# Optimization experiments

Measured on AMD Instinct MI355X. Metric: run time of the kernel, lower is better.

## Reference

```python
import jax, jax.numpy as jnp
import numpy as np

B, T, D, H, C = 32, 160, 512, 256, 6625  # batch, time, feat, gru hidden, num classes


def _gru_scan(x_proj, rk, rbias):
    """Keras GRU (reset_after=True) over time.
    x_proj: [T, B, 3H] = x @ kernel + input_bias (precomputed).
    rk: [H, 3H] recurrent kernel, rbias: [3H] recurrent bias.
    Returns hidden states [T, B, H]."""
    h0 = jnp.zeros((x_proj.shape[1], rk.shape[0]), dtype=x_proj.dtype)

    def step(h, xp):
        inner = h @ rk + rbias                 # [B, 3H]
        xz, xr, xh = jnp.split(xp, 3, axis=-1)
        rz, rr, rh = jnp.split(inner, 3, axis=-1)
        z = jax.nn.sigmoid(xz + rz)            # update gate
        r = jax.nn.sigmoid(xr + rr)            # reset gate
        hh = jnp.tanh(xh + r * rh)             # candidate
        hn = z * h + (1.0 - z) * hh
        return hn, hn

    _, hs = jax.lax.scan(step, h0, x_proj)
    return hs  # [T, B, H]


def setup_inputs() -> dict:
    key = jax.random.key(0)
    ks = jax.random.split(key, 9)
    s_in, s_rec, s_cls = 1.0 / np.sqrt(D), 1.0 / np.sqrt(H), 0.1
    return {
        "x": jax.random.normal(ks[0], (B, T, D), jnp.float32),
        "kernel_fwd": jax.random.normal(ks[1], (D, 3 * H), jnp.float32) * s_in,
        "rk_fwd": jax.random.normal(ks[2], (H, 3 * H), jnp.float32) * s_rec,
        "bias_fwd": jnp.zeros((2, 3 * H), jnp.float32),
        "kernel_bwd": jax.random.normal(ks[3], (D, 3 * H), jnp.float32) * s_in,
        "rk_bwd": jax.random.normal(ks[4], (H, 3 * H), jnp.float32) * s_rec,
        "bias_bwd": jnp.zeros((2, 3 * H), jnp.float32),
        "W": jax.random.truncated_normal(ks[5], -2.0, 2.0, (2 * H, C), jnp.float32) * s_cls,
        "b": jnp.zeros((C,), jnp.float32),
    }


def reference(x, kernel_fwd, rk_fwd, bias_fwd, kernel_bwd, rk_bwd, bias_bwd, W, b):
    x_t = jnp.transpose(x, (1, 0, 2))                       # [T, B, D]
    # forward direction
    xp_f = x_t @ kernel_fwd + bias_fwd[0]                   # [T, B, 3H]
    h_f = _gru_scan(xp_f, rk_fwd, bias_fwd[1])              # [T, B, H]
    # backward direction: run on time-reversed input, reverse output
    x_rev = x_t[::-1]
    xp_b = x_rev @ kernel_bwd + bias_bwd[0]
    h_b = _gru_scan(xp_b, rk_bwd, bias_bwd[1])[::-1]        # [T, B, H]
    out = jnp.concatenate([h_f, h_b], axis=-1)              # [T, B, 2H]
    # classifier applied per position; original reshape/matmul/reshape/transpose
    # ([B,T,2H]->[-1,2H]@W -> [B,T,C] -> [T,B,C]) is equivalent to this:
    logits = out @ W + b                                    # [T, B, C]
    return logits
```

## Files before the change

### kernel.cpp

```cpp
#include <hip/hip_runtime.h>
#include <hip/hip_bf16.h>


#define B 32
#define T 160
#define D 512
#define H 256
#define C 6625
#define H3 768
#define NT16 416
#define KP_PER_DIR 393216
#define RKB_PER_DIR 196608

typedef __attribute__((ext_vector_type(8))) short short8v;
typedef __attribute__((ext_vector_type(4))) float float4v;

__device__ inline unsigned short f2bf(float v) {
    __hip_bfloat16 b = __float2bfloat16(v);
    return *reinterpret_cast<unsigned short*>(&b);
}
__device__ inline float bf2f(unsigned short u) {
    return __uint_as_float((unsigned int)u << 16);
}

__global__ __launch_bounds__(256) void pack_rkB_kernel(
    const float* __restrict__ rkf, const float* __restrict__ rkb,
    unsigned short* __restrict__ rkB)
{
    const int idx = blockIdx.x * 256 + threadIdx.x;
    const int dir = blockIdx.y;
    const float* rk = dir ? rkb : rkf;
    const int i   = idx & 7;
    const int col = (idx >> 3) & 15;
    const int kc  = (idx >> 7) & 31;
    const int nt  = idx >> 12;
    rkB[dir * RKB_PER_DIR + idx] = f2bf(rk[(kc * 8 + i) * H3 + nt * 16 + col]);
}

__global__ __launch_bounds__(256) void pack_W_kernel(
    const float* __restrict__ W, unsigned short* __restrict__ Wp)
{
    const int idx = blockIdx.x * 256 + threadIdx.x;
    const int i   = idx & 7;
    const int col = (idx >> 3) & 15;
    const int kc  = (idx >> 7) & 63;
    const int nt  = idx >> 13;
    const int k = kc * 8 + i;
    const int c = nt * 16 + col;
    const float v = (c < C) ? W[k * C + c] : 0.f;
    Wp[idx] = f2bf(v);
}

__global__ __launch_bounds__(256) void pack_xb_kernel(
    const float* __restrict__ x, unsigned short* __restrict__ xb)
{
    const int idx = blockIdx.x * 256 + threadIdx.x;
    const int k   = idx & 511;
    const int row = idx >> 9;
    const int t   = row >> 5;
    const int b   = row & 31;
    xb[idx] = f2bf(x[(b * T + t) * 512 + k]);
}

__global__ __launch_bounds__(256) void pack_kern_kernel(
    const float* __restrict__ kf, const float* __restrict__ kb,
    unsigned short* __restrict__ kernP)
{
    const int idx = blockIdx.x * 256 + threadIdx.x;
    const int dir = blockIdx.y;
    const float* kern = dir ? kb : kf;
    const int i   = idx & 7;
    const int col = (idx >> 3) & 15;
    const int kc  = (idx >> 7) & 63;
    const int nt  = idx >> 13;
    kernP[dir * KP_PER_DIR + idx] = f2bf(kern[(kc * 8 + i) * H3 + nt * 16 + col]);
}

__global__ __launch_bounds__(256) void proj_mfma_kernel(
    const unsigned short* __restrict__ xb,
    const unsigned short* __restrict__ kernP,
    const float* __restrict__ bias_f,
    const float* __restrict__ bias_b,
    unsigned short* __restrict__ xpb)
{
    const int bid = blockIdx.x;
    const int ct  = bid / 40;
    const int rt  = bid % 40;
    const int dir = blockIdx.y;
    const int lane = threadIdx.x & 63;
    const int wid  = threadIdx.x >> 6;
    const int wm = wid >> 1, wn = wid & 1;
    const int rowBase = rt * 128 + wm * 64;
    const int lrow = lane & 15;
    const int lk8  = lane >> 4;
    const float* bias = dir ? bias_b : bias_f;

    float4v acc[4][4];
#pragma unroll
    for (int i = 0; i < 4; ++i)
#pragma unroll
        for (int k = 0; k < 4; ++k) acc[i][k] = (float4v){0.f, 0.f, 0.f, 0.f};

    const short* A  = (const short*)xb;
    const short* Bp = (const short*)(kernP + dir * KP_PER_DIR);
    const int ntBase = ct * 8 + wn * 4;

    int arow[4];
#pragma unroll
    for (int mt = 0; mt < 4; ++mt) {
        const int r0 = rowBase + mt * 16;
        const int s  = r0 >> 5;
        arow[mt] = (dir ? (159 - s) : s) * 32 + (r0 & 31);
    }

    for (int k0 = 0; k0 < 512; k0 += 32) {
        short8v aF[4], bF[4];
#pragma unroll
        for (int mt = 0; mt < 4; ++mt)
            aF[mt] = *(const short8v*)&A[(arow[mt] + lrow) * 512 + k0 + lk8 * 8];
#pragma unroll
        for (int ntw = 0; ntw < 4; ++ntw)
            bF[ntw] = *(const short8v*)&Bp[((ntBase + ntw) * 64 + (k0 >> 3) + lk8) * 128 + lrow * 8];
#pragma unroll
        for (int mt = 0; mt < 4; ++mt)
#pragma unroll
            for (int ntw = 0; ntw < 4; ++ntw)
                acc[mt][ntw] = __builtin_amdgcn_mfma_f32_16x16x32_bf16(
                    aF[mt], bF[ntw], acc[mt][ntw], 0, 0, 0);
    }

    const int orow = (lane >> 4) * 4;
#pragma unroll
    for (int ntw = 0; ntw < 4; ++ntw) {
        const int c = (ntBase + ntw) * 16 + lrow;
        const float bc = bias[c];
#pragma unroll
        for (int mt = 0; mt < 4; ++mt)
#pragma unroll
            for (int v = 0; v < 4; ++v)
                xpb[(size_t)(dir * 5120 + rowBase + mt * 16 + orow + v) * H3 + c]
                    = f2bf(acc[mt][ntw][v] + bc);
    }
}

__global__ __launch_bounds__(768, 3) void gru_scan_v6(
    const unsigned short* __restrict__ xpb,
    const unsigned short* __restrict__ rkB,
    const float* __restrict__ bias_f,
    const float* __restrict__ bias_b,
    __hip_bfloat16* __restrict__ hcatb)
{
    const int bid = blockIdx.x;
    const int dir = bid >> 5;
    const int b   = bid & 31;
    const int tid = threadIdx.x;
    const int wv  = tid >> 6;
    const int lane = tid & 63;
    const int lrow = lane & 15;
    const int lk8  = lane >> 4;
    const int j   = tid & 255;
    const float* bias = dir ? bias_b : bias_f;
    const short* Bp = (const short*)(rkB + (size_t)dir * RKB_PER_DIR);

    short8v bw[32];
#pragma unroll
    for (int i = 0; i < 4; ++i)
#pragma unroll
        for (int kk = 0; kk < 8; ++kk)
            bw[i * 8 + kk] = *(const short8v*)
                &Bp[(((wv * 4 + i) * 32) + kk * 4 + lk8) * 128 + lrow * 8];

    float rbz = 0.f, rbr = 0.f, rbh = 0.f;
    if (tid < 256) {
        rbz = bias[H3 + j];
        rbr = bias[H3 + 256 + j];
        rbh = bias[H3 + 512 + j];
    }

    __shared__ float hfp[256];
    __shared__ __align__(16) unsigned short hus[256];
    __shared__ float sums[768];
    if (tid < 256) { hfp[tid] = 0.f; hus[tid] = 0; }
    __syncthreads();

    for (int s = 0; s < T; ++s) {
        float xz = 0.f, xr = 0.f, xh = 0.f;
        if (tid < 256) {
            const unsigned short* xrow = xpb + ((size_t)(dir * T + s) * B + b) * H3;
            xz = bf2f(xrow[j]);
            xr = bf2f(xrow[256 + j]);
            xh = bf2f(xrow[512 + j]);
        }

        float4v a0 = {0.f,0.f,0.f,0.f}, a1 = {0.f,0.f,0.f,0.f};
        float4v a2 = {0.f,0.f,0.f,0.f}, a3 = {0.f,0.f,0.f,0.f};
#pragma unroll
        for (int kk = 0; kk < 8; ++kk) {
            short8v aF = *(const short8v*)&hus[kk * 32 + lk8 * 8];
            a0 = __builtin_amdgcn_mfma_f32_16x16x32_bf16(aF, bw[0 * 8 + kk], a0, 0, 0, 0);
            a1 = __builtin_amdgcn_mfma_f32_16x16x32_bf16(aF, bw[1 * 8 + kk], a1, 0, 0, 0);
            a2 = __builtin_amdgcn_mfma_f32_16x16x32_bf16(aF, bw[2 * 8 + kk], a2, 0, 0, 0);
            a3 = __builtin_amdgcn_mfma_f32_16x16x32_bf16(aF, bw[3 * 8 + kk], a3, 0, 0, 0);
        }
        if (lane < 16) {
            sums[(wv * 4 + 0) * 16 + lane] = a0[0];
            sums[(wv * 4 + 1) * 16 + lane] = a1[0];
            sums[(wv * 4 + 2) * 16 + lane] = a2[0];
            sums[(wv * 4 + 3) * 16 + lane] = a3[0];
        }
        __syncthreads();

        if (tid < 256) {
            const float sz = sums[j];
            const float sr = sums[256 + j];
            const float sh = sums[512 + j];
            const float z  = 1.f / (1.f + __expf(-(xz + sz + rbz)));
            const float r  = 1.f / (1.f + __expf(-(xr + sr + rbr)));
            const float pre = xh + r * (sh + rbh);
            const float e2  = __expf(2.f * pre);
            const float hh  = 1.f - 2.f / (e2 + 1.f);
            const float hn  = z * hfp[j] + (1.f - z) * hh;
            hfp[j] = hn;
            hus[j] = f2bf(hn);
            const int ta = dir ? (T - 1 - s) : s;
            hcatb[(ta * B + b) * 512 + dir * 256 + j] = __float2bfloat16(hn);
        }
        __syncthreads();
    }
}

__global__ __launch_bounds__(256) void cls_mfma2_kernel(
    const unsigned short* __restrict__ hcatb,
    const unsigned short* __restrict__ Wp,
    const float* __restrict__ bias,
    float* __restrict__ out)
{
    const int bid = blockIdx.x;
    const int ctn = bid / 40;
    const int rt  = bid % 40;
    const int tid = threadIdx.x;
    const int lane = tid & 63;
    const int wid  = tid >> 6;
    const int wm = wid >> 1, wn = wid & 1;
    const int lrow = lane & 15;
    const int lk8  = lane >> 4;
    const int r0   = rt * 128;

    __shared__ __align__(16) unsigned short As[128 * 512];

    {
        const uint4* src = (const uint4*)hcatb;
        for (int it = 0; it < 32; ++it) {
            const int v   = it * 256 + tid;
            const int row = v >> 6;
            const int c16 = (v & 63) << 4;
            const uint4 d = src[(size_t)(r0 + row) * 64 + (v & 63)];
            *(uint4*)((char*)As + row * 1024 + (c16 ^ ((row & 7) << 4))) = d;
        }
    }
    __syncthreads();

    float4v acc[4][8];
#pragma unroll
    for (int i = 0; i < 4; ++i)
#pragma unroll
        for (int k = 0; k < 8; ++k) acc[i][k] = (float4v){0.f, 0.f, 0.f, 0.f};

    const short* Bp = (const short*)Wp;
    const int ntBase = ctn * 16 + wn * 8;

    for (int k0 = 0; k0 < 512; k0 += 32) {
        short8v aF[4], bF[8];
#pragma unroll
        for (int mt = 0; mt < 4; ++mt) {
            const int row = wm * 64 + mt * 16 + lrow;
            const int cb  = (k0 * 2 + lk8 * 16) ^ ((row & 7) << 4);
            aF[mt] = *(const short8v*)((const char*)As + row * 1024 + cb);
        }
#pragma unroll
        for (int ntw = 0; ntw < 8; ++ntw)
            bF[ntw] = *(const short8v*)&Bp[((ntBase + ntw) * 64 + (k0 >> 3) + lk8) * 128 + lrow * 8];
#pragma unroll
        for (int mt = 0; mt < 4; ++mt)
#pragma unroll
            for (int ntw = 0; ntw < 8; ++ntw)
                acc[mt][ntw] = __builtin_amdgcn_mfma_f32_16x16x32_bf16(
                    aF[mt], bF[ntw], acc[mt][ntw], 0, 0, 0);
    }

    const int orow = (lane >> 4) * 4;
#pragma unroll
    for (int ntw = 0; ntw < 8; ++ntw) {
        const int c = (ntBase + ntw) * 16 + lrow;
        if (c >= C) continue;
        const float bc = bias[c];
#pragma unroll
        for (int mt = 0; mt < 4; ++mt)
#pragma unroll
            for (int v = 0; v < 4; ++v)
                out[(size_t)(r0 + wm * 64 + mt * 16 + orow + v) * C + c]
                    = acc[mt][ntw][v] + bc;
    }
}

__global__ __launch_bounds__(256) void proj_kernel(
    const float* __restrict__ x, const float* __restrict__ kf,
    const float* __restrict__ kb, const float* __restrict__ bias_f,
    const float* __restrict__ bias_b, float* __restrict__ xp)
{
    const int ct  = blockIdx.x;
    const int s   = blockIdx.y;
    const int dir = blockIdx.z;
    const int tid = threadIdx.x;
    const int t   = dir ? (T - 1 - s) : s;
    const float* kern = dir ? kb : kf;
    const float* bias = dir ? bias_b : bias_f;

    __shared__ float xs[32 * 512];
    for (int it = 0; it < 16; ++it) {
        int v = it * 256 + tid, row = v >> 7, k4 = v & 127;
        *(float4*)&xs[(row << 9) + (k4 << 2)] =
            *(const float4*)&x[((row * T + t) << 9) + (k4 << 2)];
    }
    __syncthreads();

    const int col = ct * 256 + tid;
    float acc[32];
#pragma unroll
    for (int r = 0; r < 32; ++r) acc[r] = 0.f;
    for (int k = 0; k < 512; k += 4) {
        float w0 = kern[(k + 0) * H3 + col];
        float w1 = kern[(k + 1) * H3 + col];
        float w2 = kern[(k + 2) * H3 + col];
        float w3 = kern[(k + 3) * H3 + col];
#pragma unroll
        for (int r = 0; r < 32; ++r) {
            float4 xv = *(const float4*)&xs[(r << 9) + k];
            acc[r] += xv.x * w0 + xv.y * w1 + xv.z * w2 + xv.w * w3;
        }
    }
    const float bb = bias[col];
    for (int r = 0; r < 32; ++r)
        xp[((dir * T + s) * B + r) * H3 + col] = acc[r] + bb;
}

__global__ __launch_bounds__(1024) void gru_scan_f32(
    const float* __restrict__ xp,
    const float* __restrict__ rk_f, const float* __restrict__ rk_b,
    const float* __restrict__ bias_f, const float* __restrict__ bias_b,
    float* __restrict__ hcat)
{
    const int bid = blockIdx.x;
    const int dir = bid >> 5;
    const int b   = bid & 31;
    const int tid = threadIdx.x;
    const int kg  = tid >> 8;
    const int j   = tid & 255;
    const int k0  = kg << 6;
    const float* rk   = dir ? rk_b : rk_f;
    const float* bias = dir ? bias_b : bias_f;
    const float rbz = bias[H3 + j];
    const float rbr = bias[H3 + 256 + j];
    const float rbh = bias[H3 + 512 + j];

    __shared__ float h[256];
    __shared__ float part[3][4][256];
    if (tid < 256) h[tid] = 0.f;
    __syncthreads();

    for (int s = 0; s < T; ++s) {
        const float* xrow = xp + ((dir * T + s) * B + b) * H3;
        float az = 0.f, ar = 0.f, ah = 0.f;
#pragma unroll 4
        for (int k = k0; k < k0 + 64; k += 4) {
            float4 h4 = *(const float4*)&h[k];
            const float* rkp = rk + k * H3 + j;
            az += h4.x * rkp[0];       ar += h4.x * rkp[256];       ah += h4.x * rkp[512];
            az += h4.y * rkp[H3];      ar += h4.y * rkp[H3+256];    ah += h4.y * rkp[H3+512];
            az += h4.z * rkp[2*H3];    ar += h4.z * rkp[2*H3+256];  ah += h4.z * rkp[2*H3+512];
            az += h4.w * rkp[3*H3];    ar += h4.w * rkp[3*H3+256];  ah += h4.w * rkp[3*H3+512];
        }
        part[0][kg][j] = az; part[1][kg][j] = ar; part[2][kg][j] = ah;
        __syncthreads();
        if (tid < 256) {
            const float sz = part[0][0][tid]+part[0][1][tid]+part[0][2][tid]+part[0][3][tid];
            const float sr = part[1][0][tid]+part[1][1][tid]+part[1][2][tid]+part[1][3][tid];
            const float sh = part[2][0][tid]+part[2][1][tid]+part[2][2][tid]+part[2][3][tid];
            const float xz = xrow[tid], xr = xrow[256+tid], xh = xrow[512+tid];
            const float z  = 1.f / (1.f + __expf(-(xz + sz + rbz)));
            const float r  = 1.f / (1.f + __expf(-(xr + sr + rbr)));
            const float pre = xh + r * (sh + rbh);
            const float e2  = __expf(2.f * pre);
            const float hh  = 1.f - 2.f / (e2 + 1.f);
            const float hn  = z * h[tid] + (1.f - z) * hh;
            h[tid] = hn;
            const int ta = dir ? (T - 1 - s) : s;
            hcat[(ta * B + b) * (2 * H) + dir * H + tid] = hn;
        }
        __syncthreads();
    }
}

__global__ __launch_bounds__(256) void cls_f32_kernel(
    const float* __restrict__ hcat, const float* __restrict__ W,
    const float* __restrict__ bias, float* __restrict__ out)
{
    const int bid = blockIdx.x;
    const int ct  = bid / 160;
    const int rt  = bid % 160;
    const int tid = threadIdx.x;
    const int r0  = rt * 32;

    __shared__ float hs[32 * 512];
    for (int it = 0; it < 16; ++it) {
        int v = it * 256 + tid, row = v >> 7, k4 = v & 127;
        *(float4*)&hs[(row << 9) + (k4 << 2)] =
            *(const float4*)&hcat[((r0 + row) << 9) + (k4 << 2)];
    }
    __syncthreads();

    const int c0 = ct * 512 + tid;
    const int c1 = c0 + 256;
    const bool v1 = (c1 < C);
    float acc0[32], acc1[32];
#pragma unroll
    for (int r = 0; r < 32; ++r) { acc0[r] = 0.f; acc1[r] = 0.f; }
    for (int k = 0; k < 512; k += 4) {
        const float* wp = W + k * C;
        float w00 = wp[c0], w01 = wp[C+c0], w02 = wp[2*C+c0], w03 = wp[3*C+c0];
        float w10 = v1 ? wp[c1] : 0.f, w11 = v1 ? wp[C+c1] : 0.f;
        float w12 = v1 ? wp[2*C+c1] : 0.f, w13 = v1 ? wp[3*C+c1] : 0.f;
#pragma unroll
        for (int r = 0; r < 32; ++r) {
            float4 hv = *(const float4*)&hs[(r << 9) + k];
            acc0[r] += hv.x*w00 + hv.y*w01 + hv.z*w02 + hv.w*w03;
            acc1[r] += hv.x*w10 + hv.y*w11 + hv.z*w12 + hv.w*w13;
        }
    }
    const float b0 = bias[c0];
    const float b1 = v1 ? bias[c1] : 0.f;
    for (int r = 0; r < 32; ++r) {
        out[(size_t)(r0+r)*C + c0] = acc0[r] + b0;
        if (v1) out[(size_t)(r0+r)*C + c1] = acc1[r] + b1;
    }
}

extern "C" void kernel_launch(void* const* d_in, const int* in_sizes, int n_in,
                              void* d_out, int out_size, void* d_ws, size_t ws_size,
                              hipStream_t stream) {
    const float* x     = (const float*)d_in[0];
    const float* kf    = (const float*)d_in[1];
    const float* rkf   = (const float*)d_in[2];
    const float* biasf = (const float*)d_in[3];
    const float* kb    = (const float*)d_in[4];
    const float* rkb   = (const float*)d_in[5];
    const float* biasb = (const float*)d_in[6];
    const float* W     = (const float*)d_in[7];
    const float* bvec  = (const float*)d_in[8];
    float* out = (float*)d_out;

    const size_t rkB_bytes   = (size_t)2 * RKB_PER_DIR * 2;
    const size_t Wp_bytes    = (size_t)NT16 * 8192 * 2;
    const size_t hcatb_bytes = (size_t)T * B * 2 * H * 2;
    const size_t planA_bytes = rkB_bytes + Wp_bytes + hcatb_bytes;

    unsigned short* xpb   = (unsigned short*)out;
    unsigned short* xb    = (unsigned short*)((char*)out + (size_t)2 * 5120 * H3 * 4);
    unsigned short* kernP = (unsigned short*)((char*)xb + (size_t)5120 * 512 * 2);

    if (ws_size >= planA_bytes) {
        char* wsb = (char*)d_ws;
        unsigned short* rkB   = (unsigned short*)wsb;
        unsigned short* Wp    = (unsigned short*)(wsb + rkB_bytes);
        __hip_bfloat16* hcatb = (__hip_bfloat16*)(wsb + rkB_bytes + Wp_bytes);

        pack_rkB_kernel<<<dim3(768, 2), 256, 0, stream>>>(rkf, rkb, rkB);
        pack_W_kernel<<<13312, 256, 0, stream>>>(W, Wp);
        pack_xb_kernel<<<10240, 256, 0, stream>>>(x, xb);
        pack_kern_kernel<<<dim3(1536, 2), 256, 0, stream>>>(kf, kb, kernP);

        proj_mfma_kernel<<<dim3(240, 2), 256, 0, stream>>>(xb, kernP, biasf, biasb, xpb);

        gru_scan_v6<<<64, 768, 0, stream>>>(xpb, rkB, biasf, biasb, hcatb);

        cls_mfma2_kernel<<<1040, 256, 0, stream>>>((const unsigned short*)hcatb,
                                                   Wp, bvec, out);
    } else {
        float* xp   = out;
        float* hcat = (float*)d_ws;
        dim3 g1(3, T, 2);
        proj_kernel<<<g1, 256, 0, stream>>>(x, kf, kb, biasf, biasb, xp);
        gru_scan_f32<<<64, 1024, 0, stream>>>(xp, rkf, rkb, biasf, biasb, hcat);
        cls_f32_kernel<<<13 * 160, 256, 0, stream>>>(hcat, W, bvec, out);
    }
}
```

Baseline: 319.2 us.

## Remap GRU scan so each wave owns all three gates for its columns

Reorganizes the recurrent scan from 12 waves to 8 waves. Each wave computes the z, r and candidate accumulators for the same 32 hidden units, so gate math reads MFMA accumulators directly. This removes the shared-memory sums buffer and one block barrier per timestep, and keeps the hidden state in registers. It raises per-wave register use and MFMA count. With a single barrier per step, writes to the shared bf16 hidden vector may race with other waves still reading it.

```diff
diff --git a/kernel.cpp b/kernel.cpp
--- a/kernel.cpp
+++ b/kernel.cpp
@@ -143,7 +143,7 @@
     }
 }
 
-__global__ __launch_bounds__(768, 3) void gru_scan_v6(
+__global__ __launch_bounds__(512, 2) void gru_scan_v7(
     const unsigned short* __restrict__ xpb,
     const unsigned short* __restrict__ rkB,
     const float* __restrict__ bias_f,
@@ -158,72 +158,74 @@
     const int lane = tid & 63;
     const int lrow = lane & 15;
     const int lk8  = lane >> 4;
-    const int j   = tid & 255;
     const float* bias = dir ? bias_b : bias_f;
     const short* Bp = (const short*)(rkB + (size_t)dir * RKB_PER_DIR);
 
-    short8v bw[32];
-#pragma unroll
-    for (int i = 0; i < 4; ++i)
-#pragma unroll
-        for (int kk = 0; kk < 8; ++kk)
-            bw[i * 8 + kk] = *(const short8v*)
-                &Bp[(((wv * 4 + i) * 32) + kk * 4 + lk8) * 128 + lrow * 8];
-
-    float rbz = 0.f, rbr = 0.f, rbh = 0.f;
-    if (tid < 256) {
-        rbz = bias[H3 + j];
-        rbr = bias[H3 + 256 + j];
-        rbh = bias[H3 + 512 + j];
-    }
-
-    __shared__ float hfp[256];
+    short8v bw[6][8];
+#pragma unroll
+    for (int g = 0; g < 3; ++g)
+#pragma unroll
+        for (int i = 0; i < 2; ++i)
+#pragma unroll
+            for (int kk = 0; kk < 8; ++kk)
+                bw[g * 2 + i][kk] = *(const short8v*)
+                    &Bp[((g * 16 + 2 * wv + i) * 32 + kk * 4 + lk8) * 128 + lrow * 8];
+
+    const int c0 = wv * 32 + lrow;
+    const int c1 = c0 + 16;
+    float rb[3][2];
+#pragma unroll
+    for (int g = 0; g < 3; ++g) {
+        rb[g][0] = bias[H3 + g * 256 + c0];
+        rb[g][1] = bias[H3 + g * 256 + c1];
+    }
+    float h0 = 0.f, h1 = 0.f;
+
     __shared__ __align__(16) unsigned short hus[256];
-    __shared__ float sums[768];
-    if (tid < 256) { hfp[tid] = 0.f; hus[tid] = 0; }
+    if (tid < 256) hus[tid] = 0;
     __syncthreads();
 
     for (int s = 0; s < T; ++s) {
-        float xz = 0.f, xr = 0.f, xh = 0.f;
-        if (tid < 256) {
-            const unsigned short* xrow = xpb + ((size_t)(dir * T + s) * B + b) * H3;
-            xz = bf2f(xrow[j]);
-            xr = bf2f(xrow[256 + j]);
-            xh = bf2f(xrow[512 + j]);
-        }
-
-        float4v a0 = {0.f,0.f,0.f,0.f}, a1 = {0.f,0.f,0.f,0.f};
-        float4v a2 = {0.f,0.f,0.f,0.f}, a3 = {0.f,0.f,0.f,0.f};
+        const unsigned short* xrow = xpb + ((size_t)(dir * T + s) * B + b) * H3;
+        float xg[3][2];
+        if (lane < 16) {
+#pragma unroll
+            for (int g = 0; g < 3; ++g) {
+                xg[g][0] = bf2f(xrow[g * 256 + c0]);
+                xg[g][1] = bf2f(xrow[g * 256 + c1]);
+            }
+        }
+
+        float4v acc[6];
+#pragma unroll
+        for (int i = 0; i < 6; ++i) acc[i] = (float4v){0.f, 0.f, 0.f, 0.f};
 #pragma unroll
         for (int kk = 0; kk < 8; ++kk) {
             short8v aF = *(const short8v*)&hus[kk * 32 + lk8 * 8];
-            a0 = __builtin_amdgcn_mfma_f32_16x16x32_bf16(aF, bw[0 * 8 + kk], a0, 0, 0, 0);
-            a1 = __builtin_amdgcn_mfma_f32_16x16x32_bf16(aF, bw[1 * 8 + kk], a1, 0, 0, 0);
-            a2 = __builtin_amdgcn_mfma_f32_16x16x32_bf16(aF, bw[2 * 8 + kk], a2, 0, 0, 0);
-            a3 = __builtin_amdgcn_mfma_f32_16x16x32_bf16(aF, bw[3 * 8 + kk], a3, 0, 0, 0);
-        }
+#pragma unroll
+            for (int i = 0; i < 6; ++i)
+                acc[i] = __builtin_amdgcn_mfma_f32_16x16x32_bf16(aF, bw[i][kk], acc[i], 0, 0, 0);
+        }
+
         if (lane < 16) {
-            sums[(wv * 4 + 0) * 16 + lane] = a0[0];
-            sums[(wv * 4 + 1) * 16 + lane] = a1[0];
-            sums[(wv * 4 + 2) * 16 + lane] = a2[0];
-            sums[(wv * 4 + 3) * 16 + lane] = a3[0];
-        }
-        __syncthreads();
-
-        if (tid < 256) {
-            const float sz = sums[j];
-            const float sr = sums[256 + j];
-            const float sh = sums[512 + j];
-            const float z  = 1.f / (1.f + __expf(-(xz + sz + rbz)));
-            const float r  = 1.f / (1.f + __expf(-(xr + sr + rbr)));
-            const float pre = xh + r * (sh + rbh);
-            const float e2  = __expf(2.f * pre);
-            const float hh  = 1.f - 2.f / (e2 + 1.f);
-            const float hn  = z * hfp[j] + (1.f - z) * hh;
-            hfp[j] = hn;
-            hus[j] = f2bf(hn);
+            const float z0 = 1.f / (1.f + __expf(-(xg[0][0] + acc[0][0] + rb[0][0])));
+            const float z1 = 1.f / (1.f + __expf(-(xg[0][1] + acc[1][0] + rb[0][1])));
+            const float r0 = 1.f / (1.f + __expf(-(xg[1][0] + acc[2][0] + rb[1][0])));
+            const float r1 = 1.f / (1.f + __expf(-(xg[1][1] + acc[3][0] + rb[1][1])));
+            const float p0 = xg[2][0] + r0 * (acc[4][0] + rb[2][0]);
+            const float p1 = xg[2][1] + r1 * (acc[5][0] + rb[2][1]);
+            const float e0 = __expf(2.f * p0);
+            const float e1 = __expf(2.f * p1);
+            const float t0 = 1.f - 2.f / (e0 + 1.f);
+            const float t1 = 1.f - 2.f / (e1 + 1.f);
+            h0 = z0 * h0 + (1.f - z0) * t0;
+            h1 = z1 * h1 + (1.f - z1) * t1;
+            hus[c0] = f2bf(h0);
+            hus[c1] = f2bf(h1);
             const int ta = dir ? (T - 1 - s) : s;
-            hcatb[(ta * B + b) * 512 + dir * 256 + j] = __float2bfloat16(hn);
+            __hip_bfloat16* hrow = hcatb + (size_t)(ta * B + b) * 512 + dir * 256;
+            hrow[c0] = __float2bfloat16(h0);
+            hrow[c1] = __float2bfloat16(h1);
         }
         __syncthreads();
     }
@@ -481,7 +483,7 @@
 
         proj_mfma_kernel<<<dim3(240, 2), 256, 0, stream>>>(xb, kernP, biasf, biasb, xpb);
 
-        gru_scan_v6<<<64, 768, 0, stream>>>(xpb, rkB, biasf, biasb, hcatb);
+        gru_scan_v7<<<64, 512, 0, stream>>>(xpb, rkB, biasf, biasb, hcatb);
 
         cls_mfma2_kernel<<<1040, 256, 0, stream>>>((const unsigned short*)hcatb,
                                                    Wp, bvec, out);
```

After: 368.0 us. 1.15x slower.
